# Kernel optimization log

Measured on AMD Instinct MI355X. Metric: run time of the kernel, lower is better.

Reference implementation:

```python
import jax, jax.numpy as jnp
import numpy as np
from jax import lax

B, V_ECC, V_ERR, T, C = 8192, 16, 12, 25, 32
F_IN = C * T           # 800 = temporal_out * tf_num
G = 64                 # gcn_out
H2 = 256               # hidden_size * 2
EHR_DIM, EHR_OUT = 64, 64

def _lhat(V):
    # bidirectional ring graph; PyG ChebConv sym-norm with lambda_max=2.0:
    # L_hat = (2/lmax) * (I - D^-1/2 A D^-1/2) - I = -D^-1/2 A D^-1/2
    i = np.arange(V)
    src = np.concatenate([i, (i + 1) % V])
    dst = np.concatenate([(i + 1) % V, i])
    A = np.zeros((V, V), np.float32)
    A[src, dst] = 1.0
    deg = A.sum(1)
    dinv = np.where(deg > 0, deg ** -0.5, 0.0).astype(np.float32)
    return jnp.asarray(-(dinv[:, None] * A * dinv[None, :]))

LHAT_ECC = _lhat(V_ECC)
LHAT_ERR = _lhat(V_ERR)

def setup_inputs():
    key = jax.random.key(0)
    ks = jax.random.split(key, 23)
    n = lambda k, s: jax.random.normal(k, s, jnp.float32) * 0.02
    return {
        "ecc": jax.random.normal(ks[0], (B, V_ECC, T), jnp.float32),
        "err": jax.random.normal(ks[1], (B, V_ERR, T), jnp.float32),
        "ehr": jax.random.normal(ks[2], (B, EHR_DIM), jnp.float32),
        "wt_ecc": n(ks[3], (C, 1, 3)), "bt_ecc": n(ks[4], (C,)),
        "wt_err": n(ks[5], (C, 1, 3)), "bt_err": n(ks[6], (C,)),
        "W0_ecc": n(ks[7], (F_IN, G)), "W1_ecc": n(ks[8], (F_IN, G)), "b_ecc": n(ks[9], (G,)),
        "W0_err": n(ks[10], (F_IN, G)), "W1_err": n(ks[11], (F_IN, G)), "b_err": n(ks[12], (G,)),
        "Wp_ecc": n(ks[13], (V_ECC * G, H2)), "bp_ecc": n(ks[14], (H2,)),
        "Wp_err": n(ks[15], (V_ERR * G, H2)), "bp_err": n(ks[16], (H2,)),
        "Wa": n(ks[17], (H2, 1)), "ba": n(ks[18], (1,)),
        "We": n(ks[19], (EHR_DIM, EHR_OUT)), "be": n(ks[20], (EHR_OUT,)),
        "Wf2": n(ks[21], (H2 + EHR_OUT, 1)), "bf2": n(ks[22], (1,)),
    }

def _temporal(x, w, b):
    # x: [B, V, T]; Conv1d(1 -> C, k=3, padding=1) per node, then flatten (C, T)
    bb, v, t = x.shape
    y = lax.conv_general_dilated(x.reshape(bb * v, 1, t), w, (1,), "SAME",
                                 dimension_numbers=("NCH", "OIH", "NCH"))
    y = y + b[None, :, None]
    return y.reshape(bb, v, -1)        # [B, V, C*T]

def _cheb(x, lhat, w0, w1, b):
    # K=2 ChebConv: out = T0(x)@W0 + T1(x)@W1 + b, T1 = L_hat x (batched over B)
    tx1 = jnp.einsum("uv,bvd->bud", lhat, x)
    return x @ w0 + tx1 @ w1 + b

def reference(ecc, err, ehr, wt_ecc, bt_ecc, wt_err, bt_err,
              W0_ecc, W1_ecc, b_ecc, W0_err, W1_err, b_err,
              Wp_ecc, bp_ecc, Wp_err, bp_err, Wa, ba, We, be, Wf2, bf2):
    bsz = ecc.shape[0]
    ecc_f = _temporal(ecc, wt_ecc, bt_ecc)                    # [B,16,800]
    err_f = _temporal(err, wt_err, bt_err)                    # [B,12,800]
    ecc_out = _cheb(ecc_f, LHAT_ECC, W0_ecc, W1_ecc, b_ecc)   # [B,16,64]
    err_out = _cheb(err_f, LHAT_ERR, W0_err, W1_err, b_err)   # [B,12,64]
    ecc_g = ecc_out.reshape(bsz, -1) @ Wp_ecc + bp_ecc        # [B,256]
    err_g = err_out.reshape(bsz, -1) @ Wp_err + bp_err        # [B,256]
    attn = jax.nn.sigmoid(jnp.tanh(ecc_g + err_g) @ Wa + ba)  # [B,1]
    fused = attn * ecc_g + (1.0 - attn) * err_g
    ehr_p = jax.nn.relu(ehr @ We + be)                        # dropout = identity (eval)
    combined = jnp.concatenate([fused, ehr_p], axis=1)        # [B,320]
    x = jax.nn.relu(combined)
    return jax.nn.sigmoid(x @ Wf2 + bf2)                      # [B,1]
```

## Files before the change

### kernel.cpp

```cpp
#include <hip/hip_runtime.h>
#include <math.h>

#define B_TOT 8192
#define KE 400
#define KR 300
#define MEP 416
#define MRP 320

#define SXE_LD 424
#define SXR_LD 328
#define SEH_LD 72
#define GE_LD 260
#define EP_LD 68

#define OFF_WEFF0E 0
#define OFF_WEFF1E 1600
#define OFF_WEFF0R 3200
#define OFF_WEFF1R 4800
#define OFF_CVE    6400
#define OFF_CVR    6464
#define OFF_BE     6528
#define OFF_BR     6784
#define U_AET 14080
#define U_ART (U_AET + 256 * MEP)
#define U_WET (U_ART + 256 * MRP)

typedef __attribute__((ext_vector_type(8))) short short8;
typedef __attribute__((ext_vector_type(4))) float floatx4;

__device__ __forceinline__ float sigmoidf_(float x) { return 1.f / (1.f + __expf(-x)); }
__device__ __forceinline__ float tanhf_(float x) { float e = __expf(2.f * x); return (e - 1.f) / (e + 1.f); }
__device__ __forceinline__ unsigned short f2bf(float x) {
    unsigned u = __float_as_uint(x);
    u += 0x7fffu + ((u >> 16) & 1u);
    return (unsigned short)(u >> 16);
}

__global__ __launch_bounds__(256) void fold_temporal(
    const float* __restrict__ wt_ecc, const float* __restrict__ bt_ecc,
    const float* __restrict__ wt_err, const float* __restrict__ bt_err,
    const float* __restrict__ W0_ecc, const float* __restrict__ W1_ecc, const float* __restrict__ b_ecc,
    const float* __restrict__ W0_err, const float* __restrict__ W1_err, const float* __restrict__ b_err,
    float* __restrict__ ws)
{
    const int blk = blockIdx.x;
    const int tid = threadIdx.x;
    const int cq = tid >> 6;
    const int g  = tid & 63;

    __shared__ float red[4][64];

    if (blk < 100) {
        const int m = blk / 25;
        const int tin = blk % 25;
        const bool is_err = (m >= 2);
        const float* wt = is_err ? wt_err : wt_ecc;
        const float* W = (m & 1) ? (is_err ? W1_err : W1_ecc) : (is_err ? W0_err : W0_ecc);
        const int t0 = tin > 0 ? tin - 1 : 0;
        const int t1 = tin < 24 ? tin + 1 : 24;
        float s = 0.f;
        #pragma unroll
        for (int c8 = 0; c8 < 8; ++c8) {
            const int c = cq * 8 + c8;
            for (int t = t0; t <= t1; ++t) {
                const int k = tin - t + 1;
                s = fmaf(wt[c * 3 + k], W[(c * 25 + t) * 64 + g], s);
            }
        }
        red[cq][g] = s;
        __syncthreads();
        if (tid < 64)
            ws[m * 1600 + tin * 64 + g] = red[0][g] + red[1][g] + red[2][g] + red[3][g];
    } else if (blk < 102) {
        const bool is_err = (blk == 101);
        const float* bt = is_err ? bt_err : bt_ecc;
        const float* W0 = is_err ? W0_err : W0_ecc;
        const float* W1 = is_err ? W1_err : W1_ecc;
        const float* bb = is_err ? b_err : b_ecc;
        float s = 0.f;
        #pragma unroll
        for (int c8 = 0; c8 < 8; ++c8) {
            const int c = cq * 8 + c8;
            const float btc = bt[c];
            #pragma unroll
            for (int t = 0; t < 25; ++t) {
                const int ct = (c * 25 + t) * 64 + g;
                s = fmaf(btc, W0[ct] - W1[ct], s);
            }
        }
        red[cq][g] = s;
        __syncthreads();
        if (tid < 64)
            ws[(is_err ? OFF_CVR : OFF_CVE) + g] =
                bb[g] + red[0][g] + red[1][g] + red[2][g] + red[3][g];
    } else {
        ws[OFF_BE + tid] = 0.f;
        ws[OFF_BR + tid] = 0.f;
    }
}

__global__ __launch_bounds__(256) void fold_graph(
    const float* __restrict__ Wp_ecc, const float* __restrict__ bp_ecc,
    const float* __restrict__ Wp_err, const float* __restrict__ bp_err,
    const float* __restrict__ We,
    float* __restrict__ wsf, unsigned short* __restrict__ wsu)
{
    const int blk = blockIdx.x;
    const int h = threadIdx.x;

    if (blk < MEP) {
        const int k = blk;
        float s = 0.f;
        if (k < KE) {
            const int v = k / 25, tin = k % 25;
            const int vp = (v + 1) & 15, vm = (v + 15) & 15;
            const float* w0 = wsf + OFF_WEFF0E + tin * 64;
            const float* w1 = wsf + OFF_WEFF1E + tin * 64;
            #pragma unroll 4
            for (int g = 0; g < 64; ++g) {
                s = fmaf(w0[g], Wp_ecc[(v * 64 + g) * 256 + h], s);
                s = fmaf(-0.5f * w1[g], Wp_ecc[(vp * 64 + g) * 256 + h] + Wp_ecc[(vm * 64 + g) * 256 + h], s);
            }
        }
        wsu[U_AET + (size_t)h * MEP + k] = f2bf(s);
    } else if (blk < MEP + MRP) {
        const int k = blk - MEP;
        float s = 0.f;
        if (k < KR) {
            const int v = k / 25, tin = k % 25;
            const int vp = (v + 1) % 12, vm = (v + 11) % 12;
            const float* w0 = wsf + OFF_WEFF0R + tin * 64;
            const float* w1 = wsf + OFF_WEFF1R + tin * 64;
            #pragma unroll 4
            for (int g = 0; g < 64; ++g) {
                s = fmaf(w0[g], Wp_err[(v * 64 + g) * 256 + h], s);
                s = fmaf(-0.5f * w1[g], Wp_err[(vp * 64 + g) * 256 + h] + Wp_err[(vm * 64 + g) * 256 + h], s);
            }
        }
        wsu[U_ART + (size_t)h * MRP + k] = f2bf(s);
    } else if (blk < MEP + MRP + 16) {
        const int i = blk - (MEP + MRP);
        const float* cv = wsf + OFF_CVE;
        float s = (i == 0) ? bp_ecc[h] : 0.f;
        #pragma unroll 4
        for (int jj = 0; jj < 64; ++jj) {
            const int j = i * 64 + jj;
            s = fmaf(cv[j & 63], Wp_ecc[(size_t)j * 256 + h], s);
        }
        atomicAdd(&wsf[OFF_BE + h], s);
    } else if (blk < MEP + MRP + 32) {
        const int i = blk - (MEP + MRP + 16);
        const float* cv = wsf + OFF_CVR;
        float s = (i == 0) ? bp_err[h] : 0.f;
        if (i < 12) {
            #pragma unroll 4
            for (int jj = 0; jj < 64; ++jj) {
                const int j = i * 64 + jj;
                s = fmaf(cv[j & 63], Wp_err[(size_t)j * 256 + h], s);
            }
        }
        atomicAdd(&wsf[OFF_BR + h], s);
    } else {
        for (int it = 0; it < 16; ++it) {
            const int idx = it * 256 + h;
            const int e = idx >> 6, d = idx & 63;
            wsu[U_WET + e * 64 + d] = f2bf(We[d * 64 + e]);
        }
    }
}

__global__ __launch_bounds__(256) void fused_main(
    const float* __restrict__ ecc, const float* __restrict__ err, const float* __restrict__ ehr,
    const float* __restrict__ wsf, const unsigned short* __restrict__ wsu,
    const float* __restrict__ Wa, const float* __restrict__ ba,
    const float* __restrict__ be_, const float* __restrict__ Wf2, const float* __restrict__ bf2,
    float* __restrict__ out)
{
    const unsigned short* awt_e = wsu + U_AET;
    const unsigned short* awt_r = wsu + U_ART;
    const unsigned short* wet   = wsu + U_WET;
    const float* biasE = wsf + OFF_BE;
    const float* biasR = wsf + OFF_BR;

    __shared__ __align__(16) char smem[32 * GE_LD * 4 * 2 + 32 * EP_LD * 4];
    unsigned short* sxe = (unsigned short*)smem;
    unsigned short* sxr = sxe + 32 * SXE_LD;
    unsigned short* seh = sxr + 32 * SXR_LD;
    float* ge = (float*)smem;
    float* gr = ge + 32 * GE_LD;
    float* ep = gr + 32 * GE_LD;

    const int tid = threadIdx.x;
    const int row0 = blockIdx.x * 32;

    for (int it = 0; it < 14; ++it) {
        const int f = it * 256 + tid;
        if (f < 32 * 106) {
            const int r = f / 106, q = f - r * 106;
            float4 v = make_float4(0.f, 0.f, 0.f, 0.f);
            if (q < 100) v = *(const float4*)(ecc + (size_t)(row0 + r) * KE + q * 4);
            const unsigned p0 = (unsigned)f2bf(v.x) | ((unsigned)f2bf(v.y) << 16);
            const unsigned p1 = (unsigned)f2bf(v.z) | ((unsigned)f2bf(v.w) << 16);
            *(uint2*)&sxe[r * SXE_LD + q * 4] = make_uint2(p0, p1);
        }
    }
    for (int it = 0; it < 11; ++it) {
        const int f = it * 256 + tid;
        if (f < 32 * 82) {
            const int r = f / 82, q = f - r * 82;
            float4 v = make_float4(0.f, 0.f, 0.f, 0.f);
            if (q < 75) v = *(const float4*)(err + (size_t)(row0 + r) * KR + q * 4);
            const unsigned p0 = (unsigned)f2bf(v.x) | ((unsigned)f2bf(v.y) << 16);
            const unsigned p1 = (unsigned)f2bf(v.z) | ((unsigned)f2bf(v.w) << 16);
            *(uint2*)&sxr[r * SXR_LD + q * 4] = make_uint2(p0, p1);
        }
    }
    for (int it = 0; it < 2; ++it) {
        const int f = it * 256 + tid;
        const int r = f >> 4, q = f & 15;
        const float4 v = *(const float4*)(ehr + (size_t)(row0 + r) * 64 + q * 4);
        const unsigned p0 = (unsigned)f2bf(v.x) | ((unsigned)f2bf(v.y) << 16);
        const unsigned p1 = (unsigned)f2bf(v.z) | ((unsigned)f2bf(v.w) << 16);
        *(uint2*)&seh[r * SEH_LD + q * 4] = make_uint2(p0, p1);
    }
    __syncthreads();

    const int wv = tid >> 6, lane = tid & 63;
    const int lm = lane & 15, lq = lane >> 4;
    const int n0 = wv * 64;

    floatx4 accE[2][4], accR[2][4], accH[2];
    #pragma unroll
    for (int mt = 0; mt < 2; ++mt) {
        accH[mt] = (floatx4){0.f, 0.f, 0.f, 0.f};
        #pragma unroll
        for (int nt = 0; nt < 4; ++nt) {
            accE[mt][nt] = (floatx4){0.f, 0.f, 0.f, 0.f};
            accR[mt][nt] = (floatx4){0.f, 0.f, 0.f, 0.f};
        }
    }

    #pragma unroll
    for (int kc = 0; kc < 2; ++kc) {
        const short8 b = *(const short8*)(wet + (wv * 16 + lm) * 64 + kc * 32 + lq * 8);
        #pragma unroll
        for (int mt = 0; mt < 2; ++mt) {
            const short8 a = *(const short8*)&seh[(mt * 16 + lm) * SEH_LD + kc * 32 + lq * 8];
            accH[mt] = __builtin_amdgcn_mfma_f32_16x16x32_bf16(a, b, accH[mt], 0, 0, 0);
        }
    }
    #pragma unroll
    for (int kc = 0; kc < 13; ++kc) {
        const short8 a0 = *(const short8*)&sxe[lm * SXE_LD + kc * 32 + lq * 8];
        const short8 a1 = *(const short8*)&sxe[(16 + lm) * SXE_LD + kc * 32 + lq * 8];
        #pragma unroll
        for (int nt = 0; nt < 4; ++nt) {
            const short8 b = *(const short8*)(awt_e + (size_t)(n0 + nt * 16 + lm) * MEP + kc * 32 + lq * 8);
            accE[0][nt] = __builtin_amdgcn_mfma_f32_16x16x32_bf16(a0, b, accE[0][nt], 0, 0, 0);
            accE[1][nt] = __builtin_amdgcn_mfma_f32_16x16x32_bf16(a1, b, accE[1][nt], 0, 0, 0);
        }
    }
    #pragma unroll
    for (int kc = 0; kc < 10; ++kc) {
        const short8 a0 = *(const short8*)&sxr[lm * SXR_LD + kc * 32 + lq * 8];
        const short8 a1 = *(const short8*)&sxr[(16 + lm) * SXR_LD + kc * 32 + lq * 8];
        #pragma unroll
        for (int nt = 0; nt < 4; ++nt) {
            const short8 b = *(const short8*)(awt_r + (size_t)(n0 + nt * 16 + lm) * MRP + kc * 32 + lq * 8);
            accR[0][nt] = __builtin_amdgcn_mfma_f32_16x16x32_bf16(a0, b, accR[0][nt], 0, 0, 0);
            accR[1][nt] = __builtin_amdgcn_mfma_f32_16x16x32_bf16(a1, b, accR[1][nt], 0, 0, 0);
        }
    }
    __syncthreads();

    #pragma unroll
    for (int mt = 0; mt < 2; ++mt) {
        #pragma unroll
        for (int nt = 0; nt < 4; ++nt) {
            #pragma unroll
            for (int rg = 0; rg < 4; ++rg) {
                const int rr = mt * 16 + lq * 4 + rg;
                const int cc = n0 + nt * 16 + lm;
                ge[rr * GE_LD + cc] = accE[mt][nt][rg];
                gr[rr * GE_LD + cc] = accR[mt][nt][rg];
            }
        }
        #pragma unroll
        for (int rg = 0; rg < 4; ++rg) {
            const int rr = mt * 16 + lq * 4 + rg;
            const int e = wv * 16 + lm;
            ep[rr * EP_LD + e] = fmaxf(accH[mt][rg] + be_[e], 0.f);
        }
    }
    __syncthreads();

    const int r = tid >> 3, i = tid & 7;
    float pa = 0.f;
    #pragma unroll 4
    for (int j = 0; j < 32; ++j) {
        const int hh = j * 8 + i;
        const float ev = ge[r * GE_LD + hh] + biasE[hh];
        const float rv = gr[r * GE_LD + hh] + biasR[hh];
        pa += tanhf_(ev + rv) * Wa[hh];
    }
    pa += __shfl_xor(pa, 1, 64); pa += __shfl_xor(pa, 2, 64); pa += __shfl_xor(pa, 4, 64);
    const float at = sigmoidf_(pa + ba[0]);
    const float om = 1.f - at;

    float po = 0.f;
    #pragma unroll 4
    for (int j = 0; j < 32; ++j) {
        const int hh = j * 8 + i;
        const float ev = ge[r * GE_LD + hh] + biasE[hh];
        const float rv = gr[r * GE_LD + hh] + biasR[hh];
        po += fmaxf(at * ev + om * rv, 0.f) * Wf2[hh];
    }
    #pragma unroll
    for (int j = 0; j < 8; ++j) {
        const int e2 = j * 8 + i;
        po += ep[r * EP_LD + e2] * Wf2[256 + e2];
    }
    po += __shfl_xor(po, 1, 64); po += __shfl_xor(po, 2, 64); po += __shfl_xor(po, 4, 64);
    if (i == 0) out[row0 + r] = sigmoidf_(po + bf2[0]);
}

extern "C" void kernel_launch(void* const* d_in, const int* in_sizes, int n_in,
                              void* d_out, int out_size, void* d_ws, size_t ws_size,
                              hipStream_t stream)
{
    (void)in_sizes; (void)n_in; (void)out_size; (void)ws_size;
    const float* ecc    = (const float*)d_in[0];
    const float* err    = (const float*)d_in[1];
    const float* ehr    = (const float*)d_in[2];
    const float* wt_ecc = (const float*)d_in[3];
    const float* bt_ecc = (const float*)d_in[4];
    const float* wt_err = (const float*)d_in[5];
    const float* bt_err = (const float*)d_in[6];
    const float* W0_ecc = (const float*)d_in[7];
    const float* W1_ecc = (const float*)d_in[8];
    const float* b_ecc  = (const float*)d_in[9];
    const float* W0_err = (const float*)d_in[10];
    const float* W1_err = (const float*)d_in[11];
    const float* b_err  = (const float*)d_in[12];
    const float* Wp_ecc = (const float*)d_in[13];
    const float* bp_ecc = (const float*)d_in[14];
    const float* Wp_err = (const float*)d_in[15];
    const float* bp_err = (const float*)d_in[16];
    const float* Wa     = (const float*)d_in[17];
    const float* ba     = (const float*)d_in[18];
    const float* We     = (const float*)d_in[19];
    const float* be     = (const float*)d_in[20];
    const float* Wf2    = (const float*)d_in[21];
    const float* bf2    = (const float*)d_in[22];
    float* wsf = (float*)d_ws;
    unsigned short* wsu = (unsigned short*)d_ws;
    float* out = (float*)d_out;

    fold_temporal<<<dim3(103), dim3(256), 0, stream>>>(
        wt_ecc, bt_ecc, wt_err, bt_err, W0_ecc, W1_ecc, b_ecc, W0_err, W1_err, b_err, wsf);
    fold_graph<<<dim3(MEP + MRP + 32 + 1), dim3(256), 0, stream>>>(
        Wp_ecc, bp_ecc, Wp_err, bp_err, We, wsf, wsu);
    fused_main<<<dim3(B_TOT / 32), dim3(256), 0, stream>>>(
        ecc, err, ehr, wsf, wsu, Wa, ba, be, Wf2, bf2, out);
}
```

Before: 155.6 us.

## Reduce epilogue in registers via shuffles instead of staging GEMM outputs in LDS

The epilogue no longer writes the full 32x256 ecc/err projection tiles and EHR outputs to shared memory. Attention and final-output dot products are now computed straight from MFMA accumulator registers, using cross-lane shuffles and a small per-wave partial-sum buffer. This shrinks the shared-memory footprint to the input staging buffers only, and launch bounds now request 3 blocks per SM to raise occupancy. In exchange it adds extra barriers and a tighter register budget that could cause spills.

Result: faster. 149.5 us (median of 2 runs) (-3.9%).

```diff
diff --git a/kernel.cpp b/kernel.cpp
--- a/kernel.cpp
+++ b/kernel.cpp
@@ -10,8 +10,6 @@
 #define SXE_LD 424
 #define SXR_LD 328
 #define SEH_LD 72
-#define GE_LD 260
-#define EP_LD 68
 
 #define OFF_WEFF0E 0
 #define OFF_WEFF1E 1600
@@ -169,7 +167,7 @@
     }
 }
 
-__global__ __launch_bounds__(256) void fused_main(
+__global__ __launch_bounds__(256, 3) void fused_main(
     const float* __restrict__ ecc, const float* __restrict__ err, const float* __restrict__ ehr,
     const float* __restrict__ wsf, const unsigned short* __restrict__ wsu,
     const float* __restrict__ Wa, const float* __restrict__ ba,
@@ -182,13 +180,13 @@
     const float* biasE = wsf + OFF_BE;
     const float* biasR = wsf + OFF_BR;
 
-    __shared__ __align__(16) char smem[32 * GE_LD * 4 * 2 + 32 * EP_LD * 4];
+    __shared__ __align__(16) char smem[32 * SXE_LD * 2 + 32 * SXR_LD * 2 + 32 * SEH_LD * 2];
     unsigned short* sxe = (unsigned short*)smem;
     unsigned short* sxr = sxe + 32 * SXE_LD;
     unsigned short* seh = sxr + 32 * SXR_LD;
-    float* ge = (float*)smem;
-    float* gr = ge + 32 * GE_LD;
-    float* ep = gr + 32 * GE_LD;
+    float* pa_part = (float*)smem;
+    float* at_arr  = pa_part + 128;
+    float* po_part = at_arr + 32;
 
     const int tid = threadIdx.x;
     const int row0 = blockIdx.x * 32;
@@ -271,57 +269,77 @@
             accR[1][nt] = __builtin_amdgcn_mfma_f32_16x16x32_bf16(a1, b, accR[1][nt], 0, 0, 0);
         }
     }
-    __syncthreads();
-
-    #pragma unroll
-    for (int mt = 0; mt < 2; ++mt) {
-        #pragma unroll
-        for (int nt = 0; nt < 4; ++nt) {
-            #pragma unroll
-            for (int rg = 0; rg < 4; ++rg) {
-                const int rr = mt * 16 + lq * 4 + rg;
-                const int cc = n0 + nt * 16 + lm;
-                ge[rr * GE_LD + cc] = accE[mt][nt][rg];
-                gr[rr * GE_LD + cc] = accR[mt][nt][rg];
-            }
-        }
+
+    float bE[4], bR[4], wa[4], wf[4];
+    #pragma unroll
+    for (int nt = 0; nt < 4; ++nt) {
+        const int h = n0 + nt * 16 + lm;
+        bE[nt] = biasE[h]; bR[nt] = biasR[h]; wa[nt] = Wa[h]; wf[nt] = Wf2[h];
+    }
+    const int e_lane = wv * 16 + lm;
+    const float eh_be = be_[e_lane];
+    const float eh_wf = Wf2[256 + e_lane];
+
+    float pa_lane[2][4];
+    #pragma unroll
+    for (int mt = 0; mt < 2; ++mt)
         #pragma unroll
         for (int rg = 0; rg < 4; ++rg) {
-            const int rr = mt * 16 + lq * 4 + rg;
-            const int e = wv * 16 + lm;
-            ep[rr * EP_LD + e] = fmaxf(accH[mt][rg] + be_[e], 0.f);
-        }
-    }
-    __syncthreads();
-
-    const int r = tid >> 3, i = tid & 7;
-    float pa = 0.f;
-    #pragma unroll 4
-    for (int j = 0; j < 32; ++j) {
-        const int hh = j * 8 + i;
-        const float ev = ge[r * GE_LD + hh] + biasE[hh];
-        const float rv = gr[r * GE_LD + hh] + biasR[hh];
-        pa += tanhf_(ev + rv) * Wa[hh];
-    }
-    pa += __shfl_xor(pa, 1, 64); pa += __shfl_xor(pa, 2, 64); pa += __shfl_xor(pa, 4, 64);
-    const float at = sigmoidf_(pa + ba[0]);
-    const float om = 1.f - at;
-
-    float po = 0.f;
-    #pragma unroll 4
-    for (int j = 0; j < 32; ++j) {
-        const int hh = j * 8 + i;
-        const float ev = ge[r * GE_LD + hh] + biasE[hh];
-        const float rv = gr[r * GE_LD + hh] + biasR[hh];
-        po += fmaxf(at * ev + om * rv, 0.f) * Wf2[hh];
-    }
-    #pragma unroll
-    for (int j = 0; j < 8; ++j) {
-        const int e2 = j * 8 + i;
-        po += ep[r * EP_LD + e2] * Wf2[256 + e2];
-    }
-    po += __shfl_xor(po, 1, 64); po += __shfl_xor(po, 2, 64); po += __shfl_xor(po, 4, 64);
-    if (i == 0) out[row0 + r] = sigmoidf_(po + bf2[0]);
+            float s = 0.f;
+            #pragma unroll
+            for (int nt = 0; nt < 4; ++nt) {
+                const float ev = accE[mt][nt][rg] + bE[nt];
+                const float rv = accR[mt][nt][rg] + bR[nt];
+                s = fmaf(tanhf_(ev + rv), wa[nt], s);
+            }
+            s += __shfl_xor(s, 1, 64); s += __shfl_xor(s, 2, 64);
+            s += __shfl_xor(s, 4, 64); s += __shfl_xor(s, 8, 64);
+            pa_lane[mt][rg] = s;
+        }
+
+    __syncthreads();
+    if (lm == 0) {
+        #pragma unroll
+        for (int mt = 0; mt < 2; ++mt)
+            #pragma unroll
+            for (int rg = 0; rg < 4; ++rg)
+                pa_part[wv * 32 + mt * 16 + lq * 4 + rg] = pa_lane[mt][rg];
+    }
+    __syncthreads();
+    if (tid < 32)
+        at_arr[tid] = sigmoidf_(pa_part[tid] + pa_part[32 + tid] + pa_part[64 + tid] + pa_part[96 + tid] + ba[0]);
+    __syncthreads();
+
+    float po_lane[2][4];
+    #pragma unroll
+    for (int mt = 0; mt < 2; ++mt)
+        #pragma unroll
+        for (int rg = 0; rg < 4; ++rg) {
+            const int r = mt * 16 + lq * 4 + rg;
+            const float at = at_arr[r];
+            const float om = 1.f - at;
+            float s = 0.f;
+            #pragma unroll
+            for (int nt = 0; nt < 4; ++nt) {
+                const float ev = accE[mt][nt][rg] + bE[nt];
+                const float rv = accR[mt][nt][rg] + bR[nt];
+                s = fmaf(fmaxf(at * ev + om * rv, 0.f), wf[nt], s);
+            }
+            s = fmaf(fmaxf(accH[mt][rg] + eh_be, 0.f), eh_wf, s);
+            s += __shfl_xor(s, 1, 64); s += __shfl_xor(s, 2, 64);
+            s += __shfl_xor(s, 4, 64); s += __shfl_xor(s, 8, 64);
+            po_lane[mt][rg] = s;
+        }
+    if (lm == 0) {
+        #pragma unroll
+        for (int mt = 0; mt < 2; ++mt)
+            #pragma unroll
+            for (int rg = 0; rg < 4; ++rg)
+                po_part[wv * 32 + mt * 16 + lq * 4 + rg] = po_lane[mt][rg];
+    }
+    __syncthreads();
+    if (tid < 32)
+        out[row0 + tid] = sigmoidf_(po_part[tid] + po_part[32 + tid] + po_part[64 + tid] + po_part[96 + tid] + bf2[0]);
 }
 
 extern "C" void kernel_launch(void* const* d_in, const int* in_sizes, int n_in,
```
